# Kernel optimization log

Measured on AMD Instinct MI355X. Metric: run time of the kernel, lower is better.

## Reference

```python
import jax, jax.numpy as jnp
import numpy as np

B = 1048576
INDIM = 10
DIM = 32
LAYERS = 4
MODES = DIM // 2 + 1  # 17 rfft modes


def setup_inputs() -> dict:
    key = jax.random.key(0)
    ks = jax.random.split(key, 10)
    scale = 1.0 / (DIM * DIM)
    inp = {
        "x": jax.random.normal(ks[0], (B, INDIM), dtype=jnp.float32),
        # stem: Linear(indim, dim), stored as [in, out]
        "stem_W": jax.random.normal(ks[1], (INDIM, DIM), dtype=jnp.float32) / np.sqrt(INDIM),
        "stem_b": jnp.zeros((DIM,), dtype=jnp.float32),
        # per-layer complex spectral weights, stored as real/imag parts [L, modes, modes]
        "fno_wr": scale * jax.random.uniform(ks[2], (LAYERS, MODES, MODES), dtype=jnp.float32),
        "fno_wi": scale * jax.random.uniform(ks[3], (LAYERS, MODES, MODES), dtype=jnp.float32),
        # per-layer proj: Linear(dim, dim), stored as [L, in, out]
        "proj_W": jax.random.normal(ks[4], (LAYERS, DIM, DIM), dtype=jnp.float32) / np.sqrt(DIM),
        "proj_b": jnp.zeros((LAYERS, DIM), dtype=jnp.float32),
        # head: Linear(dim, indim)
        "head_W": jax.random.normal(ks[5], (DIM, INDIM), dtype=jnp.float32) / np.sqrt(DIM),
        "head_b": jnp.zeros((INDIM,), dtype=jnp.float32),
    }
    return inp


def reference(x, stem_W, stem_b, fno_wr, fno_wi, proj_W, proj_b, head_W, head_b):
    # stem
    h = x @ stem_W + stem_b  # [B, DIM]
    for i in range(LAYERS):
        w = fno_wr[i] + 1j * fno_wi[i]  # [MODES, MODES] complex64
        hf = jnp.fft.rfft(h, axis=-1)  # [B, MODES] complex
        # complex linear mix of modes (bias=False since condition_num=0)
        x1 = jnp.fft.irfft(jnp.einsum('bi,io->bo', hf, w), axis=-1)  # [B, DIM]
        x2 = h @ proj_W[i] + proj_b[i]  # [B, DIM]
        h = jax.nn.silu(x1 + x2)
    return h @ head_W + head_b  # [B, INDIM]
```

## Files before the change

### kernel.cpp

```cpp
#include <hip/hip_runtime.h>
#include <math.h>

#define INDIM 10
#define DIM 32
#define LAYERS 4
#define MODES 17

#define LOG2E 1.4426950408889634f
#define LN2   0.6931471805599453f

#define WS_FRAG_OFF 0
#define WS_BIAS_OFF 11264

typedef _Float16 f16;
typedef _Float16 f16x8 __attribute__((ext_vector_type(8)));
typedef float f32x16 __attribute__((ext_vector_type(16)));
typedef unsigned u32x2 __attribute__((ext_vector_type(2)));

union BU { f16x8 v; unsigned u[4]; };
union CU { f32x16 v; float4 q[4]; };

__global__ void fno_prep(const float* __restrict__ wr,
                         const float* __restrict__ wi,
                         const float* __restrict__ projW,
                         const float* __restrict__ stemW,
                         const float* __restrict__ headW,
                         const float* __restrict__ stemB,
                         const float* __restrict__ projB,
                         const float* __restrict__ headB,
                         f16* __restrict__ frag,
                         float* __restrict__ bias2) {
    const int l  = blockIdx.x;
    const int tx = threadIdx.x;
    const int j  = tx & 31;
    const int n  = tx >> 5;

    __shared__ float ct[32], st[32];
    if (tx < 32) {
        float ang = (2.0f * 3.14159265358979323846f / 32.0f) * (float)tx;
        ct[tx] = cosf(ang);
        st[tx] = sinf(ang);
    }
    __syncthreads();

    const float* lwr = wr + l * MODES * MODES;
    const float* lwi = wi + l * MODES * MODES;

    float acc = 0.0f;
    for (int o = 0; o < MODES; ++o) {
        float re = 0.0f, im = 0.0f;
        for (int m = 0; m < MODES; ++m) {
            int t = (m * n) & 31;
            float c = ct[t], s = st[t];
            float a = lwr[m * MODES + o];
            float b = lwi[m * MODES + o];
            re += c * a + s * b;
            im += c * b - s * a;
        }
        int t2 = (o * j) & 31;
        float f = (o == 0 || o == 16) ? 1.0f : 2.0f;
        acc += f * (re * ct[t2] - im * st[t2]);
    }
    acc = acc * (1.0f / 32.0f) + projW[(l * DIM + n) * DIM + j];

    const float wscale = (l == 0) ? LOG2E : 1.0f;
    const int kc = n >> 4;
    const int G  = (n >> 3) & 1;
    const int e  = n & 7;
    const int ln = G * 32 + j;
    frag[((l * 2 + kc) * 64 + ln) * 8 + e] = (f16)(wscale * acc);

    if (l == 0) {
        if (tx < 64) {
            const int lnn = tx;
            const int c2  = lnn & 31;
            const int G2  = lnn >> 5;
#pragma unroll
            for (int ee = 0; ee < 8; ++ee) {
                int k = 8 * G2 + ee;
                frag[(8 * 64 + lnn) * 8 + ee] =
                    (f16)(k < INDIM ? stemW[k * DIM + c2] : 0.0f);
            }
#pragma unroll
            for (int kcc = 0; kcc < 2; ++kcc)
#pragma unroll
                for (int ee = 0; ee < 8; ++ee) {
                    int k = 16 * kcc + 8 * G2 + ee;
                    frag[((9 + kcc) * 64 + lnn) * 8 + ee] =
                        (f16)(c2 < INDIM ? LN2 * headW[k * INDIM + c2] : 0.0f);
                }
        }
        if (tx < 32) {
#pragma unroll
            for (int f = 0; f < 6; ++f) {
                float v;
                if (f == 0)      v = stemB[tx];
                else if (f <= 4) v = LOG2E * projB[(f - 1) * DIM + tx];
                else             v = (tx < INDIM) ? headB[tx] : 0.0f;
                bias2[f * 32 + tx] = v;
            }
        }
    }
}

__device__ __forceinline__ float exp2_fast(float x) {
#if __has_builtin(__builtin_amdgcn_exp2f)
    return __builtin_amdgcn_exp2f(x);
#else
    return exp2f(x);
#endif
}

__device__ __forceinline__ unsigned pk2(float a, float b) {
    auto h2 = __builtin_amdgcn_cvt_pkrtz(a, b);
    return __builtin_bit_cast(unsigned, h2);
}

__device__ __forceinline__ void pswap(unsigned& a, unsigned& b) {
#if __has_builtin(__builtin_amdgcn_permlane32_swap)
    u32x2 r = __builtin_amdgcn_permlane32_swap(a, b, false, false);
    a = r[0];
    b = r[1];
#else
    asm("v_permlane32_swap_b32 %0, %1" : "+v"(a), "+v"(b));
    __builtin_amdgcn_sched_barrier(0);
#endif
}

template <bool SILU>
__device__ __forceinline__ void pack_exchange(const f32x16& D, BU& b0, BU& b1) {
    float s[16];
    if (SILU) {
        float u[16];
#pragma unroll
        for (int r = 0; r < 16; ++r) u[r] = exp2_fast(-D[r]);
#pragma unroll
        for (int r = 0; r < 16; ++r) u[r] = 1.0f + u[r];
#pragma unroll
        for (int r = 0; r < 16; ++r) u[r] = __builtin_amdgcn_rcpf(u[r]);
#pragma unroll
        for (int r = 0; r < 16; ++r) s[r] = D[r] * u[r];
    } else {
#pragma unroll
        for (int r = 0; r < 16; ++r) s[r] = D[r];
    }
    unsigned q0 = pk2(s[0],  s[1]);
    unsigned q1 = pk2(s[2],  s[3]);
    unsigned q2 = pk2(s[4],  s[5]);
    unsigned q3 = pk2(s[6],  s[7]);
    unsigned q4 = pk2(s[8],  s[9]);
    unsigned q5 = pk2(s[10], s[11]);
    unsigned q6 = pk2(s[12], s[13]);
    unsigned q7 = pk2(s[14], s[15]);
    pswap(q0, q2);
    pswap(q1, q3);
    pswap(q4, q6);
    pswap(q5, q7);
    b0.u[0] = q0; b0.u[1] = q1; b0.u[2] = q2; b0.u[3] = q3;
    b1.u[0] = q4; b1.u[1] = q5; b1.u[2] = q6; b1.u[3] = q7;
}

__device__ __forceinline__ f32x16 ld_bias(const float* sbias, int stage, int G) {
    CU c;
#pragma unroll
    for (int rq = 0; rq < 4; ++rq)
        c.q[rq] = *(const float4*)&sbias[stage * 32 + rq * 8 + G * 4];
    return c.v;
}

__device__ __forceinline__ f16x8 ld_frag(const f16* sfrag, int f, int ln) {
    return *(const f16x8*)&sfrag[(f * 64 + ln) * 8];
}

template <bool GUARD>
__device__ __forceinline__ BU load_x(const float* __restrict__ x, long rb,
                                     int c, int G, int nrows) {
    BU b;
    b.u[0] = 0; b.u[1] = 0; b.u[2] = 0; b.u[3] = 0;
    const long r = rb + c;
    if (!GUARD || r < nrows) {
        const float* xp = x + r * INDIM;
        if (G == 0) {
            float2 p0 = *(const float2*)(xp + 0);
            float2 p1 = *(const float2*)(xp + 2);
            float2 p2 = *(const float2*)(xp + 4);
            float2 p3 = *(const float2*)(xp + 6);
            b.u[0] = pk2(p0.x, p0.y);
            b.u[1] = pk2(p1.x, p1.y);
            b.u[2] = pk2(p2.x, p2.y);
            b.u[3] = pk2(p3.x, p3.y);
        } else {
            float2 p4 = *(const float2*)(xp + 8);
            b.u[0] = pk2(p4.x, p4.y);
        }
    }
    return b;
}

template <bool GUARD>
__device__ __forceinline__ void store_o(float* __restrict__ out, long rb,
                                        int c, int G, int nrows, const f32x16& Dh) {
    const long r = rb + c;
    if (!GUARD || r < nrows) {
        float* op = out + r * INDIM;
        if (G == 0) {
            *(float2*)(op + 0) = make_float2(Dh[0], Dh[1]);
            *(float2*)(op + 2) = make_float2(Dh[2], Dh[3]);
            *(float2*)(op + 8) = make_float2(Dh[4], Dh[5]);
        } else {
            *(float2*)(op + 4) = make_float2(Dh[0], Dh[1]);
            *(float2*)(op + 6) = make_float2(Dh[2], Dh[3]);
        }
    }
}

template <bool GUARD>
__global__ __launch_bounds__(256, 6) void fno_main(
    const float* __restrict__ x,
    const f16*  __restrict__ fragbuf,
    const float* __restrict__ bias2,
    float* __restrict__ out,
    int nrows) {

    __shared__ __align__(16) f16 sfrag[11 * 64 * 8];
    __shared__ __align__(16) float sbias[6 * 32];

    {
        const int tid = threadIdx.x;
        uint4* dv = (uint4*)sfrag;
        const uint4* sv = (const uint4*)fragbuf;
#pragma unroll
        for (int i = 0; i < 3; ++i) {
            int idx = tid + i * 256;
            if (idx < 704) dv[idx] = sv[idx];
        }
        if (tid < 48) ((float4*)sbias)[tid] = ((const float4*)bias2)[tid];
    }
    __syncthreads();

    const int tid = threadIdx.x;
    const int w   = tid >> 6;
    const int ln  = tid & 63;
    const int c   = ln & 31;
    const int G   = ln >> 5;

    const long rb = (long)blockIdx.x * 128 + (long)w * 32;

    BU bx = load_x<GUARD>(x, rb, c, G, nrows);
    f16x8 as = ld_frag(sfrag, 8, ln);
    f32x16 cb = ld_bias(sbias, 0, G);
    f32x16 D = __builtin_amdgcn_mfma_f32_32x32x16_f16(as, bx.v, cb, 0, 0, 0);

    BU b0, b1;
    pack_exchange<false>(D, b0, b1);

#pragma unroll
    for (int l = 0; l < LAYERS; ++l) {
        f16x8 w0 = ld_frag(sfrag, 2 * l, ln);
        f16x8 w1 = ld_frag(sfrag, 2 * l + 1, ln);
        cb = ld_bias(sbias, 1 + l, G);
        f32x16 t = __builtin_amdgcn_mfma_f32_32x32x16_f16(w0, b0.v, cb, 0, 0, 0);
        t = __builtin_amdgcn_mfma_f32_32x32x16_f16(w1, b1.v, t, 0, 0, 0);
        pack_exchange<true>(t, b0, b1);
    }

    f16x8 ah0 = ld_frag(sfrag, 9, ln);
    f16x8 ah1 = ld_frag(sfrag, 10, ln);
    cb = ld_bias(sbias, 5, G);
    f32x16 H = __builtin_amdgcn_mfma_f32_32x32x16_f16(ah0, b0.v, cb, 0, 0, 0);
    H = __builtin_amdgcn_mfma_f32_32x32x16_f16(ah1, b1.v, H, 0, 0, 0);

    store_o<GUARD>(out, rb, c, G, nrows, H);
}

extern "C" void kernel_launch(void* const* d_in, const int* in_sizes, int n_in,
                              void* d_out, int out_size, void* d_ws, size_t ws_size,
                              hipStream_t stream) {
    const float* x      = (const float*)d_in[0];
    const float* stemW  = (const float*)d_in[1];
    const float* stemB  = (const float*)d_in[2];
    const float* fno_wr = (const float*)d_in[3];
    const float* fno_wi = (const float*)d_in[4];
    const float* projW  = (const float*)d_in[5];
    const float* projB  = (const float*)d_in[6];
    const float* headW  = (const float*)d_in[7];
    const float* headB  = (const float*)d_in[8];
    float* out = (float*)d_out;

    f16*   frag  = (f16*)((char*)d_ws + WS_FRAG_OFF);
    float* bias2 = (float*)((char*)d_ws + WS_BIAS_OFF);

    const int nrows = in_sizes[0] / INDIM;

    fno_prep<<<LAYERS, 1024, 0, stream>>>(fno_wr, fno_wi, projW, stemW, headW,
                                          stemB, projB, headB, frag, bias2);

    const int rows_per_block = 128;
    const int nblk = (nrows + rows_per_block - 1) / rows_per_block;
    if (nrows % rows_per_block == 0)
        fno_main<false><<<nblk, 256, 0, stream>>>(x, frag, bias2, out, nrows);
    else
        fno_main<true><<<nblk, 256, 0, stream>>>(x, frag, bias2, out, nrows);
}
```

Before: 57.82 us.

## Share spectral partials in prep kernel, split SiLU packing, raise occupancy bound

```diff
diff --git a/kernel.cpp b/kernel.cpp
--- a/kernel.cpp
+++ b/kernel.cpp
@@ -36,6 +36,7 @@
     const int n  = tx >> 5;
 
     __shared__ float ct[32], st[32];
+    __shared__ float sre[MODES][32], sim[MODES][32];
     if (tx < 32) {
         float ang = (2.0f * 3.14159265358979323846f / 32.0f) * (float)tx;
         ct[tx] = cosf(ang);
@@ -46,20 +47,28 @@
     const float* lwr = wr + l * MODES * MODES;
     const float* lwi = wi + l * MODES * MODES;
 
-    float acc = 0.0f;
-    for (int o = 0; o < MODES; ++o) {
+    if (tx < MODES * 32) {
+        const int o  = tx >> 5;
+        const int nn = tx & 31;
         float re = 0.0f, im = 0.0f;
         for (int m = 0; m < MODES; ++m) {
-            int t = (m * n) & 31;
+            int t = (m * nn) & 31;
             float c = ct[t], s = st[t];
             float a = lwr[m * MODES + o];
             float b = lwi[m * MODES + o];
             re += c * a + s * b;
             im += c * b - s * a;
         }
+        sre[o][nn] = re;
+        sim[o][nn] = im;
+    }
+    __syncthreads();
+
+    float acc = 0.0f;
+    for (int o = 0; o < MODES; ++o) {
         int t2 = (o * j) & 31;
         float f = (o == 0 || o == 16) ? 1.0f : 2.0f;
-        acc += f * (re * ct[t2] - im * st[t2]);
+        acc += f * (sre[o][n] * ct[t2] - sim[o][n] * st[t2]);
     }
     acc = acc * (1.0f / 32.0f) + projW[(l * DIM + n) * DIM + j];
 
@@ -129,35 +138,34 @@
 
 template <bool SILU>
 __device__ __forceinline__ void pack_exchange(const f32x16& D, BU& b0, BU& b1) {
-    float s[16];
-    if (SILU) {
-        float u[16];
-#pragma unroll
-        for (int r = 0; r < 16; ++r) u[r] = exp2_fast(-D[r]);
-#pragma unroll
-        for (int r = 0; r < 16; ++r) u[r] = 1.0f + u[r];
-#pragma unroll
-        for (int r = 0; r < 16; ++r) u[r] = __builtin_amdgcn_rcpf(u[r]);
-#pragma unroll
-        for (int r = 0; r < 16; ++r) s[r] = D[r] * u[r];
-    } else {
-#pragma unroll
-        for (int r = 0; r < 16; ++r) s[r] = D[r];
-    }
-    unsigned q0 = pk2(s[0],  s[1]);
-    unsigned q1 = pk2(s[2],  s[3]);
-    unsigned q2 = pk2(s[4],  s[5]);
-    unsigned q3 = pk2(s[6],  s[7]);
-    unsigned q4 = pk2(s[8],  s[9]);
-    unsigned q5 = pk2(s[10], s[11]);
-    unsigned q6 = pk2(s[12], s[13]);
-    unsigned q7 = pk2(s[14], s[15]);
-    pswap(q0, q2);
-    pswap(q1, q3);
-    pswap(q4, q6);
-    pswap(q5, q7);
-    b0.u[0] = q0; b0.u[1] = q1; b0.u[2] = q2; b0.u[3] = q3;
-    b1.u[0] = q4; b1.u[1] = q5; b1.u[2] = q6; b1.u[3] = q7;
+    unsigned q[8];
+#pragma unroll
+    for (int h = 0; h < 2; ++h) {
+        float u[8];
+        if (SILU) {
+#pragma unroll
+            for (int r = 0; r < 8; ++r) u[r] = exp2_fast(-D[8 * h + r]);
+#pragma unroll
+            for (int r = 0; r < 8; ++r) u[r] = 1.0f + u[r];
+#pragma unroll
+            for (int r = 0; r < 8; ++r) u[r] = __builtin_amdgcn_rcpf(u[r]);
+#pragma unroll
+            for (int r = 0; r < 8; ++r) u[r] = D[8 * h + r] * u[r];
+        } else {
+#pragma unroll
+            for (int r = 0; r < 8; ++r) u[r] = D[8 * h + r];
+        }
+        q[4 * h + 0] = pk2(u[0], u[1]);
+        q[4 * h + 1] = pk2(u[2], u[3]);
+        q[4 * h + 2] = pk2(u[4], u[5]);
+        q[4 * h + 3] = pk2(u[6], u[7]);
+    }
+    pswap(q[0], q[2]);
+    pswap(q[1], q[3]);
+    pswap(q[4], q[6]);
+    pswap(q[5], q[7]);
+    b0.u[0] = q[0]; b0.u[1] = q[1]; b0.u[2] = q[2]; b0.u[3] = q[3];
+    b1.u[0] = q[4]; b1.u[1] = q[5]; b1.u[2] = q[6]; b1.u[3] = q[7];
 }
 
 __device__ __forceinline__ f32x16 ld_bias(const float* sbias, int stage, int G) {
@@ -215,7 +223,7 @@
 }
 
 template <bool GUARD>
-__global__ __launch_bounds__(256, 6) void fno_main(
+__global__ __launch_bounds__(256, 8) void fno_main(
     const float* __restrict__ x,
     const f16*  __restrict__ fragbuf,
     const float* __restrict__ bias2,
```

After: 50.11 us (median of 2 runs). 13.3% less time.
